# Kernel optimization log

Hardware: AMD Instinct MI355X
Metric: run time of the kernel (lower is better)

The kernel has to match this reference:

```python
import jax, jax.numpy as jnp
import numpy as np

B, DIM, H, W = 8, 128, 96, 96
EPS = 1e-5  # torch LayerNorm default


def setup_inputs() -> dict:
    key = jax.random.key(0)
    ks = jax.random.split(key, 4)
    d = DIM
    return {
        "x": jax.random.normal(ks[0], (B, d, H, W), jnp.float32),
        "W_in": jax.random.normal(ks[1], (2 * d, d), jnp.float32) * (d ** -0.5),
        "b_in": jnp.zeros((2 * d,), jnp.float32),
        "dw_w": jax.random.normal(ks[2], (d, 1, 7), jnp.float32) * 0.3,
        "dw_b": jnp.zeros((d,), jnp.float32),
        "gamma": jnp.ones((d,), jnp.float32),
        "beta": jnp.zeros((d,), jnp.float32),
        "W_out": jax.random.normal(ks[3], (d, d), jnp.float32) * (d ** -0.5),
        "b_out": jnp.zeros((d,), jnp.float32),
    }


def _mixer(x, W_in, b_in, dw_w, dw_b, gamma, beta, W_out, b_out):
    # x: (N, L, C). LinearStateSpace1D fallback mixer.
    d = x.shape[-1]
    uv = x @ W_in.T + b_in                      # (N, L, 2C)
    u, v = jnp.split(uv, 2, axis=-1)            # torch .chunk(2, -1)
    u = jax.nn.silu(u)
    v = jnp.swapaxes(v, 1, 2)                   # (N, C, L)
    v = jax.lax.conv_general_dilated(
        v, dw_w, window_strides=(1,), padding=[(3, 3)],
        dimension_numbers=("NCH", "OIH", "NCH"), feature_group_count=d,
    ) + dw_b[None, :, None]
    v = jax.nn.silu(jnp.swapaxes(v, 1, 2))      # (N, L, C)
    y = u * v
    mu = jnp.mean(y, axis=-1, keepdims=True)
    var = jnp.mean((y - mu) ** 2, axis=-1, keepdims=True)
    y = (y - mu) * jax.lax.rsqrt(var + EPS) * gamma + beta
    return y @ W_out.T + b_out


def reference(x, W_in, b_in, dw_w, dw_b, gamma, beta, W_out, b_out):
    Bc, C, Hh, Ww = x.shape
    L = Hh * Ww
    # 4-direction expand: lr, tb, rl (flip lr), bt (flip tb) -> stack on batch
    s_lr = jnp.transpose(x, (0, 2, 3, 1)).reshape(Bc, L, C)
    s_tb = jnp.transpose(x, (0, 3, 2, 1)).reshape(Bc, L, C)
    seqs = jnp.concatenate([s_lr, s_tb, s_lr[:, ::-1], s_tb[:, ::-1]], axis=0)
    y = _mixer(seqs, W_in, b_in, dw_w, dw_b, gamma, beta, W_out, b_out)
    y_lr, y_tb, y_rl, y_bt = jnp.split(y, 4, axis=0)
    y_rl = y_rl[:, ::-1]
    y_bt = y_bt[:, ::-1]
    m_lr = jnp.transpose(y_lr.reshape(Bc, Hh, Ww, C), (0, 3, 1, 2))
    m_rl = jnp.transpose(y_rl.reshape(Bc, Hh, Ww, C), (0, 3, 1, 2))
    m_tb = jnp.transpose(y_tb.reshape(Bc, Ww, Hh, C), (0, 3, 2, 1))
    m_bt = jnp.transpose(y_bt.reshape(Bc, Ww, Hh, C), (0, 3, 2, 1))
    return (m_lr + m_tb + m_rl + m_bt) * 0.25
```

## Files before the change

kernel.cpp:

```cpp
#include <hip/hip_runtime.h>

#define BB 8
#define HH 96
#define WW 96
#define LL 9216
#define EPSF 1e-5f

typedef __attribute__((ext_vector_type(8))) short short8;
typedef __attribute__((ext_vector_type(4))) float f32x4;
typedef __attribute__((ext_vector_type(2))) float f32x2;
typedef __attribute__((ext_vector_type(4))) unsigned int uint32x4;
typedef unsigned short ushort_t;
typedef unsigned int uint32;

__device__ __forceinline__ float silu_f(float x){
    return x * __builtin_amdgcn_rcpf(1.0f + __expf(-x));
}
__device__ __forceinline__ ushort_t f2bf(float f){
    uint32 u = __float_as_uint(f);
    u += 0x7FFFu + ((u >> 16) & 1u);
    return (ushort_t)(u >> 16);
}
__device__ __forceinline__ float bf2f(short h){
    return __uint_as_float(((uint32)(ushort_t)h) << 16);
}
__device__ __forceinline__ uint32 pack2(float a, float b){
    return (uint32)f2bf(a) | ((uint32)f2bf(b) << 16);
}

__global__ __launch_bounds__(256) void k_prep(const float* __restrict__ Win,
        const float* __restrict__ Wout, const float* __restrict__ dw_w,
        ushort_t* __restrict__ W2, ushort_t* __restrict__ WO2,
        float* __restrict__ dwT){
    int i = blockIdx.x * 256 + threadIdx.x;
    {
        int e = i & 7, ln = (i >> 3) & 63, ks = (i >> 9) & 3, of = i >> 11;
        W2[i] = f2bf(Win[(of*16 + (ln & 15))*128 + ks*32 + (ln >> 4)*8 + e]);
    }
    if (i < 16384){
        int e = i & 7, ln = (i >> 3) & 63, ks = (i >> 9) & 3, of = i >> 11;
        WO2[i] = f2bf(Wout[(of*16 + (ln & 15))*128 + ks*32 + (ln >> 4)*8 + e]);
    }
    if (i < 896){
        int j = i >> 7, c = i & 127;
        dwT[i] = dw_w[c*7 + j];
    }
}

__global__ __launch_bounds__(256) void k_gemmA(const float* __restrict__ x,
        const ushort_t* __restrict__ W2, const float* __restrict__ b_in,
        ushort_t* __restrict__ UV){
    __shared__ __align__(16) char unia[34816];
    float (*xt)[65] = (float(*)[65])unia;
    ushort_t* ec = (ushort_t*)unia;
    __shared__ __align__(16) ushort_t xtile[64 * 128];

    const int b = blockIdx.y, l0 = blockIdx.x * 64, tid = threadIdx.x;
    const int wv = tid >> 6, lane = tid & 63;
    const int lo = lane & 15, hi = lane >> 4;

    #pragma unroll
    for (int k = 0; k < 32; ++k){
        int c = (tid >> 6) + k * 4;
        xt[c][lane] = x[((size_t)(b * 128 + c)) * LL + l0 + lane];
    }
    __syncthreads();
    #pragma unroll
    for (int p = 0; p < 16; ++p){
        int l = (tid >> 6) + p * 4;
        uint32 v = pack2(xt[2 * lane][l], xt[2 * lane + 1][l]);
        *(uint32*)((char*)xtile + l * 256 + ((lane * 4) ^ ((l & 7) << 4))) = v;
    }
    __syncthreads();

    const f32x4 zero = {0.f, 0.f, 0.f, 0.f};
    f32x4 acc[4][4];
    #pragma unroll
    for (int om = 0; om < 4; ++om)
        #pragma unroll
        for (int lf = 0; lf < 4; ++lf) acc[om][lf] = zero;

    #pragma unroll
    for (int ks = 0; ks < 4; ++ks){
        short8 af[4], bfr[4];
        #pragma unroll
        for (int om = 0; om < 4; ++om)
            af[om] = *(const short8*)(W2 + (size_t)(((wv*4 + om)*4 + ks)*64 + lane)*8);
        #pragma unroll
        for (int lf = 0; lf < 4; ++lf){
            int tok = lf * 16 + lo;
            bfr[lf] = *(const short8*)((char*)xtile + tok * 256 +
                        ((ks * 64 + hi * 16) ^ ((tok & 7) << 4)));
        }
        #pragma unroll
        for (int om = 0; om < 4; ++om)
            #pragma unroll
            for (int lf = 0; lf < 4; ++lf)
                acc[om][lf] = __builtin_amdgcn_mfma_f32_16x16x32_bf16(af[om], bfr[lf], acc[om][lf], 0, 0, 0);
    }
    __syncthreads();

    #pragma unroll
    for (int om = 0; om < 4; ++om){
        int obase = wv * 64 + om * 16 + hi * 4;
        f32x4 bia = *(const f32x4*)(b_in + obase);
        const bool isU = (wv < 2);
        #pragma unroll
        for (int lf = 0; lf < 4; ++lf){
            #pragma unroll
            for (int r = 0; r < 4; ++r){
                float v = acc[om][lf][r] + bia[r];
                if (isU) v = silu_f(v);
                ec[(obase + r) * 68 + lf * 16 + lo] = f2bf(v);
            }
        }
    }
    __syncthreads();

    const int r8 = tid >> 5, c32 = tid & 31;
    #pragma unroll
    for (int p = 0; p < 32; ++p){
        int row = r8 + p * 8;
        int col = c32 * 2;
        uint32 v = *(const uint32*)(ec + row * 68 + col);
        *(uint32*)(UV + ((size_t)(b * 256 + row)) * LL + l0 + col) = v;
    }
}

__device__ __forceinline__ float tbfly8(float (&x)[8], int lane){
    const int t0 = lane & 1, t1 = (lane >> 1) & 1, t2 = (lane >> 2) & 1;
    float y[4], z[2];
    #pragma unroll
    for (int j = 0; j < 4; ++j){
        float keep = t0 ? x[2*j+1] : x[2*j];
        float send = t0 ? x[2*j]   : x[2*j+1];
        y[j] = keep + __shfl_xor(send, 1);
    }
    #pragma unroll
    for (int j = 0; j < 2; ++j){
        float keep = t1 ? y[2*j+1] : y[2*j];
        float send = t1 ? y[2*j]   : y[2*j+1];
        z[j] = keep + __shfl_xor(send, 2);
    }
    float keep = t2 ? z[1] : z[0];
    float send = t2 ? z[0] : z[1];
    return keep + __shfl_xor(send, 4);
}

__global__ __launch_bounds__(512, 4) void k_mixout(const ushort_t* __restrict__ UV,
        const float* __restrict__ dwT, const float* __restrict__ dw_b,
        const float* __restrict__ gamma, const float* __restrict__ beta,
        const ushort_t* __restrict__ WO2, const float* __restrict__ b_out,
        float* __restrict__ out){
    __shared__ __align__(16) float red[8][32][12];
    __shared__ float tot[32 * 6];
    __shared__ __align__(16) char ytile[32 * 288];

    const int flat = blockIdx.y * 288 + blockIdx.x;
    const int nf = (flat & 7) * 288 + (flat >> 3);
    const int b  = nf / 288;
    const int m0 = (nf % 288) * 32;

    const int tid  = threadIdx.x;
    const int lane = tid & 63;
    const int wv   = tid >> 6;
    const int cl   = lane & 15;
    const int tg   = lane >> 4;
    const int c0   = wv * 16 + cl;
    const int m8   = m0 + tg * 8;
    const int h    = m8 / WW;
    const int w0g  = m8 - h * WW;

    const ushort_t* vrow = UV + ((size_t)(b * 256 + 128) + c0) * LL + m8;

    short8 u8  = *(const short8*)(UV + ((size_t)(b * 256) + c0) * LL + m8);
    short8 WBm = *(const short8*)(vrow);
    short8 WA  = *(const short8*)(vrow - 8);
    short8 WC  = *(const short8*)(vrow + 8);
    short8 g8[6];
    bool inb[6];
    #pragma unroll
    for (int r = 0; r < 6; ++r){
        const int dd = (r < 3) ? (r - 3) : (r - 2);
        const int hd = h + dd;
        inb[r] = (hd >= 0) && (hd < HH);
        g8[r] = *(const short8*)(vrow + 96 * dd);
    }
    float cw[7];
    #pragma unroll
    for (int j = 0; j < 7; ++j) cw[j] = dwT[j * 128 + c0];
    const float bias = dw_b[c0];

    float ya[8], yb[8], yc[8], yd[8];
    float Sa, Qa, Sb, Qb, Sc, Qc, Sd, Qd;

    {
        float f[14];
        #pragma unroll
        for (int k = 0; k < 14; ++k){
            int e = 5 + k;
            f[k] = bf2f(e < 8 ? WA[e] : (e < 16 ? WBm[e - 8] : WC[e - 16]));
        }
        if (m8 == 0){ f[0] = 0.f; f[1] = 0.f; f[2] = 0.f; }
        if (m8 == LL - 8){ f[11] = 0.f; f[12] = 0.f; f[13] = 0.f; }
        float qa[8], qb[8];
        #pragma unroll
        for (int i = 0; i < 8; ++i){
            float caf = bias, cbw = bias;
            #pragma unroll
            for (int j = 0; j < 7; ++j){
                caf = fmaf(cw[j],     f[i + j], caf);
                cbw = fmaf(cw[6 - j], f[i + j], cbw);
            }
            float uu = bf2f(u8[i]);
            ya[i] = uu * silu_f(caf);
            yb[i] = uu * silu_f(cbw);
            qa[i] = ya[i] * ya[i];
            qb[i] = yb[i] * yb[i];
        }
        Sa = tbfly8(ya, lane); Sa += __shfl_xor(Sa, 8);
        Qa = tbfly8(qa, lane); Qa += __shfl_xor(Qa, 8);
        Sb = tbfly8(yb, lane); Sb += __shfl_xor(Sb, 8);
        Qb = tbfly8(qb, lane); Qb += __shfl_xor(Qb, 8);
    }

    {
        float caf[8], cbw[8];
        #pragma unroll
        for (int i = 0; i < 8; ++i){
            float v0 = bf2f(WBm[i]);
            caf[i] = fmaf(cw[3], v0, bias);
            cbw[i] = caf[i];
        }
        #pragma unroll
        for (int r = 0; r < 6; ++r){
            const int dd = (r < 3) ? (r - 3) : (r - 2);
            const int j  = dd + 3;
            float gv[8];
            if (inb[r]){
                #pragma unroll
                for (int i = 0; i < 8; ++i) gv[i] = bf2f(g8[r][i]);
            } else {
                const int hd = h + dd;
                const int del = (hd < 0) ? (LL - 1) : (1 - LL);
                #pragma unroll
                for (int i = 0; i < 8; ++i){
                    int q = (w0g + i) * HH + hd;
                    bool ok = (unsigned)q < (unsigned)LL;
                    gv[i] = ok ? bf2f(vrow[96 * dd + del + i]) : 0.f;
                }
            }
            #pragma unroll
            for (int i = 0; i < 8; ++i){
                caf[i] = fmaf(cw[j],     gv[i], caf[i]);
                cbw[i] = fmaf(cw[6 - j], gv[i], cbw[i]);
            }
        }
        float qc[8], qd[8];
        #pragma unroll
        for (int i = 0; i < 8; ++i){
            float uu = bf2f(u8[i]);
            yc[i] = uu * silu_f(caf[i]);
            yd[i] = uu * silu_f(cbw[i]);
            qc[i] = yc[i] * yc[i];
            qd[i] = yd[i] * yd[i];
        }
        Sc = tbfly8(yc, lane); Sc += __shfl_xor(Sc, 8);
        Qc = tbfly8(qc, lane); Qc += __shfl_xor(Qc, 8);
        Sd = tbfly8(yd, lane); Sd += __shfl_xor(Sd, 8);
        Qd = tbfly8(qd, lane); Qd += __shfl_xor(Qd, 8);
    }

    {
        const int tok32 = tg * 8 + (lane & 7);
        const int halfp = (lane >> 3) & 1;
        f32x4 stv;
        if (halfp){ stv[0] = Sc; stv[1] = Qc; stv[2] = Sd; stv[3] = Qd; }
        else      { stv[0] = Sa; stv[1] = Qa; stv[2] = Sb; stv[3] = Qb; }
        *(f32x4*)(&red[wv][tok32][halfp * 4]) = stv;
    }
    __syncthreads();
    if (tid < 32){
        f32x4 s0 = {0.f, 0.f, 0.f, 0.f}, s1 = {0.f, 0.f, 0.f, 0.f};
        #pragma unroll
        for (int w2 = 0; w2 < 8; ++w2){
            s0 += *(const f32x4*)(&red[w2][tid][0]);
            s1 += *(const f32x4*)(&red[w2][tid][4]);
        }
        const float inv = 1.f / 128.f;
        float mua = s0[0] * inv, ra = __builtin_amdgcn_rsqf(s0[1] * inv - mua * mua + EPSF);
        float mub = s0[2] * inv, rb = __builtin_amdgcn_rsqf(s0[3] * inv - mub * mub + EPSF);
        float muc = s1[0] * inv, rc = __builtin_amdgcn_rsqf(s1[1] * inv - muc * muc + EPSF);
        float mud = s1[2] * inv, rd = __builtin_amdgcn_rsqf(s1[3] * inv - mud * mud + EPSF);
        float C = mua * ra + mub * rb + muc * rc + mud * rd;
        tot[tid * 6 + 0] = ra; tot[tid * 6 + 1] = rb;
        tot[tid * 6 + 2] = rc; tot[tid * 6 + 3] = rd;
        tot[tid * 6 + 4] = C;
    }
    __syncthreads();

    {
        const float g4 = 0.25f * gamma[c0];
        const float be = beta[c0];
        #pragma unroll
        for (int i = 0; i < 8; ++i){
            int tok = tg * 8 + i;
            f32x2 r01 = *(const f32x2*)(&tot[tok * 6 + 0]);
            f32x2 r23 = *(const f32x2*)(&tot[tok * 6 + 2]);
            float C   = tot[tok * 6 + 4];
            float v = fmaf(ya[i], r01[0], fmaf(yb[i], r01[1],
                      fmaf(yc[i], r23[0], fmaf(yd[i], r23[1], -C))));
            int swz = ((tok & 7) ^ (tok >> 3)) << 4;
            *(ushort_t*)(ytile + tok * 288 + ((c0 * 2) ^ swz)) =
                f2bf(fmaf(g4, v, be));
        }
    }
    __syncthreads();

    const int lo = lane & 15, hi = lane >> 4;
    const int ow = wv;
    const f32x4 zero = {0.f, 0.f, 0.f, 0.f};
    f32x4 acc[2] = {zero, zero};
    #pragma unroll
    for (int ks = 0; ks < 4; ++ks){
        short8 af = *(const short8*)(WO2 + (size_t)((ow * 4 + ks) * 64 + lane) * 8);
        #pragma unroll
        for (int t2 = 0; t2 < 2; ++t2){
            int tok = t2 * 16 + lo;
            int swz = ((tok & 7) ^ (tok >> 3)) << 4;
            short8 bfr = *(const short8*)(ytile + tok * 288 +
                            ((ks * 64 + hi * 16) ^ swz));
            acc[t2] = __builtin_amdgcn_mfma_f32_16x16x32_bf16(af, bfr, acc[t2], 0, 0, 0);
        }
    }
    {
        f32x4 bia = *(const f32x4*)(b_out + ow * 16 + hi * 4);
        #pragma unroll
        for (int t2 = 0; t2 < 2; ++t2){
            int l = m0 + t2 * 16 + lo;
            #pragma unroll
            for (int r = 0; r < 4; ++r){
                int o = ow * 16 + hi * 4 + r;
                out[((size_t)(b * 128 + o)) * LL + l] = acc[t2][r] + bia[r];
            }
        }
    }
}

extern "C" void kernel_launch(void* const* d_in, const int* in_sizes, int n_in,
                              void* d_out, int out_size, void* d_ws, size_t ws_size,
                              hipStream_t stream) {
    const float* x     = (const float*)d_in[0];
    const float* W_in  = (const float*)d_in[1];
    const float* b_in  = (const float*)d_in[2];
    const float* dw_w  = (const float*)d_in[3];
    const float* dw_b  = (const float*)d_in[4];
    const float* gamma = (const float*)d_in[5];
    const float* beta  = (const float*)d_in[6];
    const float* W_out = (const float*)d_in[7];
    const float* b_out = (const float*)d_in[8];
    float* out = (float*)d_out;

    ushort_t* UV  = (ushort_t*)d_ws;
    ushort_t* W2  = UV + (size_t)BB * 256 * LL + 32;
    ushort_t* WO2 = W2 + 256 * 128;
    float*    dwT = (float*)(WO2 + 128 * 128);

    k_prep<<<128, 256, 0, stream>>>(W_in, W_out, dw_w, W2, WO2, dwT);

    dim3 gA(LL / 64, BB);
    k_gemmA<<<gA, 256, 0, stream>>>(x, W2, b_in, UV);

    dim3 gM(288, BB);
    k_mixout<<<gM, 512, 0, stream>>>(UV, dwT, dw_b, gamma, beta,
                                     WO2, b_out, out);
}
```

Baseline: 77.86 us.

## Remap mixout threads so each wave owns tokens, reducing LayerNorm in-wave

Each block now runs 256 threads instead of 512. Each wave handles 8 tokens across all 128 channels, with every lane processing two channels. The LayerNorm statistics are therefore reduced entirely with cross-lane shuffles, which removes the shared-memory reduction buffers and two block barriers. In exchange each thread holds twice the loaded data and accumulators, and each wave now computes two output-row MFMA tiles. The loads of UV rows become per-lane strided across channels rather than channel-contiguous, which may change coalescing behaviour. Relies on a pack2 helper presumed defined in the unseen part of the file.

```diff
diff --git a/kernel.cpp b/kernel.cpp
--- a/kernel.cpp
+++ b/kernel.cpp
@@ -147,14 +147,20 @@
     return keep + __shfl_xor(send, 4);
 }
 
-__global__ __launch_bounds__(512, 4) void k_mixout(const ushort_t* __restrict__ UV,
+__device__ __forceinline__ float wred8(float (&x)[8], int lane){
+    float s = tbfly8(x, lane);
+    s += __shfl_xor(s, 8);
+    s += __shfl_xor(s, 16);
+    s += __shfl_xor(s, 32);
+    return s;
+}
+
+__global__ __launch_bounds__(256, 3) void k_mixout(const ushort_t* __restrict__ UV,
         const float* __restrict__ dwT, const float* __restrict__ dw_b,
         const float* __restrict__ gamma, const float* __restrict__ beta,
         const ushort_t* __restrict__ WO2, const float* __restrict__ b_out,
         float* __restrict__ out){
-    __shared__ __align__(16) float red[8][32][12];
-    __shared__ float tot[32 * 6];
-    __shared__ __align__(16) char ytile[32 * 288];
+    __shared__ __align__(16) char ytile[32 * 256];
 
     const int flat = blockIdx.y * 288 + blockIdx.x;
     const int nf = (flat & 7) * 288 + (flat >> 3);
@@ -164,72 +170,70 @@
     const int tid  = threadIdx.x;
     const int lane = tid & 63;
     const int wv   = tid >> 6;
-    const int cl   = lane & 15;
-    const int tg   = lane >> 4;
-    const int c0   = wv * 16 + cl;
-    const int m8   = m0 + tg * 8;
+    const int cs   = lane;
+    const int m8   = m0 + wv * 8;
     const int h    = m8 / WW;
     const int w0g  = m8 - h * WW;
 
-    const ushort_t* vrow = UV + ((size_t)(b * 256 + 128) + c0) * LL + m8;
-
-    short8 u8  = *(const short8*)(UV + ((size_t)(b * 256) + c0) * LL + m8);
-    short8 WBm = *(const short8*)(vrow);
-    short8 WA  = *(const short8*)(vrow - 8);
-    short8 WC  = *(const short8*)(vrow + 8);
-    short8 g8[6];
+    const ushort_t* vrow[2];
+    vrow[0] = UV + ((size_t)(b * 256 + 128) + 2 * cs) * LL + m8;
+    vrow[1] = vrow[0] + LL;
+
+    short8 u8v[2], WBv[2], WAv[2], WCv[2], g8v[2][6];
+    #pragma unroll
+    for (int ch = 0; ch < 2; ++ch){
+        u8v[ch] = *(const short8*)(UV + ((size_t)(b * 256) + 2 * cs + ch) * LL + m8);
+        WBv[ch] = *(const short8*)(vrow[ch]);
+        WAv[ch] = *(const short8*)(vrow[ch] - 8);
+        WCv[ch] = *(const short8*)(vrow[ch] + 8);
+    }
     bool inb[6];
     #pragma unroll
     for (int r = 0; r < 6; ++r){
         const int dd = (r < 3) ? (r - 3) : (r - 2);
         const int hd = h + dd;
         inb[r] = (hd >= 0) && (hd < HH);
-        g8[r] = *(const short8*)(vrow + 96 * dd);
-    }
-    float cw[7];
-    #pragma unroll
-    for (int j = 0; j < 7; ++j) cw[j] = dwT[j * 128 + c0];
-    const float bias = dw_b[c0];
-
-    float ya[8], yb[8], yc[8], yd[8];
-    float Sa, Qa, Sb, Qb, Sc, Qc, Sd, Qd;
-
-    {
+        g8v[0][r] = *(const short8*)(vrow[0] + 96 * dd);
+        g8v[1][r] = *(const short8*)(vrow[1] + 96 * dd);
+    }
+    f32x2 cw2[7];
+    #pragma unroll
+    for (int j = 0; j < 7; ++j) cw2[j] = *(const f32x2*)(dwT + j * 128 + 2 * cs);
+    const f32x2 bias2 = *(const f32x2*)(dw_b + 2 * cs);
+
+    float ya[2][8], yb[2][8], yc[2][8], yd[2][8];
+
+    #pragma unroll
+    for (int ch = 0; ch < 2; ++ch){
         float f[14];
         #pragma unroll
         for (int k = 0; k < 14; ++k){
             int e = 5 + k;
-            f[k] = bf2f(e < 8 ? WA[e] : (e < 16 ? WBm[e - 8] : WC[e - 16]));
+            f[k] = bf2f(e < 8 ? WAv[ch][e] : (e < 16 ? WBv[ch][e - 8] : WCv[ch][e - 16]));
         }
         if (m8 == 0){ f[0] = 0.f; f[1] = 0.f; f[2] = 0.f; }
         if (m8 == LL - 8){ f[11] = 0.f; f[12] = 0.f; f[13] = 0.f; }
-        float qa[8], qb[8];
         #pragma unroll
         for (int i = 0; i < 8; ++i){
-            float caf = bias, cbw = bias;
+            float caf = bias2[ch], cbw = bias2[ch];
             #pragma unroll
             for (int j = 0; j < 7; ++j){
-                caf = fmaf(cw[j],     f[i + j], caf);
-                cbw = fmaf(cw[6 - j], f[i + j], cbw);
+                caf = fmaf(cw2[j][ch],     f[i + j], caf);
+                cbw = fmaf(cw2[6 - j][ch], f[i + j], cbw);
             }
-            float uu = bf2f(u8[i]);
-            ya[i] = uu * silu_f(caf);
-            yb[i] = uu * silu_f(cbw);
-            qa[i] = ya[i] * ya[i];
-            qb[i] = yb[i] * yb[i];
-        }
-        Sa = tbfly8(ya, lane); Sa += __shfl_xor(Sa, 8);
-        Qa = tbfly8(qa, lane); Qa += __shfl_xor(Qa, 8);
-        Sb = tbfly8(yb, lane); Sb += __shfl_xor(Sb, 8);
-        Qb = tbfly8(qb, lane); Qb += __shfl_xor(Qb, 8);
-    }
-
-    {
+            float uu = bf2f(u8v[ch][i]);
+            ya[ch][i] = uu * silu_f(caf);
+            yb[ch][i] = uu * silu_f(cbw);
+        }
+    }
+
+    #pragma unroll
+    for (int ch = 0; ch < 2; ++ch){
         float caf[8], cbw[8];
         #pragma unroll
         for (int i = 0; i < 8; ++i){
-            float v0 = bf2f(WBm[i]);
-            caf[i] = fmaf(cw[3], v0, bias);
+            float v0 = bf2f(WBv[ch][i]);
+            caf[i] = fmaf(cw2[3][ch], v0, bias2[ch]);
             cbw[i] = caf[i];
         }
         #pragma unroll
@@ -239,7 +243,7 @@
             float gv[8];
             if (inb[r]){
                 #pragma unroll
-                for (int i = 0; i < 8; ++i) gv[i] = bf2f(g8[r][i]);
+                for (int i = 0; i < 8; ++i) gv[i] = bf2f(g8v[ch][r][i]);
             } else {
                 const int hd = h + dd;
                 const int del = (hd < 0) ? (LL - 1) : (1 - LL);
@@ -247,102 +251,104 @@
                 for (int i = 0; i < 8; ++i){
                     int q = (w0g + i) * HH + hd;
                     bool ok = (unsigned)q < (unsigned)LL;
-                    gv[i] = ok ? bf2f(vrow[96 * dd + del + i]) : 0.f;
+                    gv[i] = ok ? bf2f(vrow[ch][96 * dd + del + i]) : 0.f;
                 }
             }
             #pragma unroll
             for (int i = 0; i < 8; ++i){
-                caf[i] = fmaf(cw[j],     gv[i], caf[i]);
-                cbw[i] = fmaf(cw[6 - j], gv[i], cbw[i]);
+                caf[i] = fmaf(cw2[j][ch],     gv[i], caf[i]);
+                cbw[i] = fmaf(cw2[6 - j][ch], gv[i], cbw[i]);
             }
         }
-        float qc[8], qd[8];
         #pragma unroll
         for (int i = 0; i < 8; ++i){
-            float uu = bf2f(u8[i]);
-            yc[i] = uu * silu_f(caf[i]);
-            yd[i] = uu * silu_f(cbw[i]);
-            qc[i] = yc[i] * yc[i];
-            qd[i] = yd[i] * yd[i];
-        }
-        Sc = tbfly8(yc, lane); Sc += __shfl_xor(Sc, 8);
-        Qc = tbfly8(qc, lane); Qc += __shfl_xor(Qc, 8);
-        Sd = tbfly8(yd, lane); Sd += __shfl_xor(Sd, 8);
-        Qd = tbfly8(qd, lane); Qd += __shfl_xor(Qd, 8);
-    }
-
+            float uu = bf2f(u8v[ch][i]);
+            yc[ch][i] = uu * silu_f(caf[i]);
+            yd[ch][i] = uu * silu_f(cbw[i]);
+        }
+    }
+
+    float Sa, Qa, Sb, Qb, Sc, Qc, Sd, Qd;
     {
-        const int tok32 = tg * 8 + (lane & 7);
-        const int halfp = (lane >> 3) & 1;
-        f32x4 stv;
-        if (halfp){ stv[0] = Sc; stv[1] = Qc; stv[2] = Sd; stv[3] = Qd; }
-        else      { stv[0] = Sa; stv[1] = Qa; stv[2] = Sb; stv[3] = Qb; }
-        *(f32x4*)(&red[wv][tok32][halfp * 4]) = stv;
-    }
-    __syncthreads();
-    if (tid < 32){
-        f32x4 s0 = {0.f, 0.f, 0.f, 0.f}, s1 = {0.f, 0.f, 0.f, 0.f};
-        #pragma unroll
-        for (int w2 = 0; w2 < 8; ++w2){
-            s0 += *(const f32x4*)(&red[w2][tid][0]);
-            s1 += *(const f32x4*)(&red[w2][tid][4]);
-        }
-        const float inv = 1.f / 128.f;
-        float mua = s0[0] * inv, ra = __builtin_amdgcn_rsqf(s0[1] * inv - mua * mua + EPSF);
-        float mub = s0[2] * inv, rb = __builtin_amdgcn_rsqf(s0[3] * inv - mub * mub + EPSF);
-        float muc = s1[0] * inv, rc = __builtin_amdgcn_rsqf(s1[1] * inv - muc * muc + EPSF);
-        float mud = s1[2] * inv, rd = __builtin_amdgcn_rsqf(s1[3] * inv - mud * mud + EPSF);
-        float C = mua * ra + mub * rb + muc * rc + mud * rd;
-        tot[tid * 6 + 0] = ra; tot[tid * 6 + 1] = rb;
-        tot[tid * 6 + 2] = rc; tot[tid * 6 + 3] = rd;
-        tot[tid * 6 + 4] = C;
-    }
-    __syncthreads();
+        float s[8], q[8];
+        #pragma unroll
+        for (int i = 0; i < 8; ++i){ s[i] = ya[0][i] + ya[1][i];
+            q[i] = fmaf(ya[0][i], ya[0][i], ya[1][i] * ya[1][i]); }
+        Sa = wred8(s, lane); Qa = wred8(q, lane);
+        #pragma unroll
+        for (int i = 0; i < 8; ++i){ s[i] = yb[0][i] + yb[1][i];
+            q[i] = fmaf(yb[0][i], yb[0][i], yb[1][i] * yb[1][i]); }
+        Sb = wred8(s, lane); Qb = wred8(q, lane);
+        #pragma unroll
+        for (int i = 0; i < 8; ++i){ s[i] = yc[0][i] + yc[1][i];
+            q[i] = fmaf(yc[0][i], yc[0][i], yc[1][i] * yc[1][i]); }
+        Sc = wred8(s, lane); Qc = wred8(q, lane);
+        #pragma unroll
+        for (int i = 0; i < 8; ++i){ s[i] = yd[0][i] + yd[1][i];
+            q[i] = fmaf(yd[0][i], yd[0][i], yd[1][i] * yd[1][i]); }
+        Sd = wred8(s, lane); Qd = wred8(q, lane);
+    }
+    const float inv = 1.f / 128.f;
+    float mua = Sa * inv, ra = __builtin_amdgcn_rsqf(Qa * inv - mua * mua + EPSF);
+    float mub = Sb * inv, rb = __builtin_amdgcn_rsqf(Qb * inv - mub * mub + EPSF);
+    float muc = Sc * inv, rc = __builtin_amdgcn_rsqf(Qc * inv - muc * muc + EPSF);
+    float mud = Sd * inv, rd = __builtin_amdgcn_rsqf(Qd * inv - mud * mud + EPSF);
+    float Cst = fmaf(mua, ra, fmaf(mub, rb, fmaf(muc, rc, mud * rd)));
 
     {
-        const float g4 = 0.25f * gamma[c0];
-        const float be = beta[c0];
+        f32x2 g2 = *(const f32x2*)(gamma + 2 * cs);
+        f32x2 e2 = *(const f32x2*)(beta + 2 * cs);
+        const float g40 = 0.25f * g2[0], g41 = 0.25f * g2[1];
         #pragma unroll
         for (int i = 0; i < 8; ++i){
-            int tok = tg * 8 + i;
-            f32x2 r01 = *(const f32x2*)(&tot[tok * 6 + 0]);
-            f32x2 r23 = *(const f32x2*)(&tot[tok * 6 + 2]);
-            float C   = tot[tok * 6 + 4];
-            float v = fmaf(ya[i], r01[0], fmaf(yb[i], r01[1],
-                      fmaf(yc[i], r23[0], fmaf(yd[i], r23[1], -C))));
+            float rai = __shfl(ra, i, 8);
+            float rbi = __shfl(rb, i, 8);
+            float rci = __shfl(rc, i, 8);
+            float rdi = __shfl(rd, i, 8);
+            float Ci  = __shfl(Cst, i, 8);
+            float v0 = fmaf(ya[0][i], rai, fmaf(yb[0][i], rbi,
+                       fmaf(yc[0][i], rci, fmaf(yd[0][i], rdi, -Ci))));
+            float v1 = fmaf(ya[1][i], rai, fmaf(yb[1][i], rbi,
+                       fmaf(yc[1][i], rci, fmaf(yd[1][i], rdi, -Ci))));
+            uint32 pk = pack2(fmaf(g40, v0, e2[0]), fmaf(g41, v1, e2[1]));
+            int tok = wv * 8 + i;
             int swz = ((tok & 7) ^ (tok >> 3)) << 4;
-            *(ushort_t*)(ytile + tok * 288 + ((c0 * 2) ^ swz)) =
-                f2bf(fmaf(g4, v, be));
+            *(uint32*)(ytile + tok * 256 + ((cs * 4) ^ swz)) = pk;
         }
     }
     __syncthreads();
 
     const int lo = lane & 15, hi = lane >> 4;
-    const int ow = wv;
     const f32x4 zero = {0.f, 0.f, 0.f, 0.f};
-    f32x4 acc[2] = {zero, zero};
+    f32x4 acc[2][2];
+    acc[0][0] = zero; acc[0][1] = zero; acc[1][0] = zero; acc[1][1] = zero;
     #pragma unroll
     for (int ks = 0; ks < 4; ++ks){
-        short8 af = *(const short8*)(WO2 + (size_t)((ow * 4 + ks) * 64 + lane) * 8);
+        short8 af[2];
+        #pragma unroll
+        for (int om = 0; om < 2; ++om)
+            af[om] = *(const short8*)(WO2 + (size_t)(((wv*2 + om)*4 + ks)*64 + lane)*8);
         #pragma unroll
         for (int t2 = 0; t2 < 2; ++t2){
             int tok = t2 * 16 + lo;
             int swz = ((tok & 7) ^ (tok >> 3)) << 4;
-            short8 bfr = *(const short8*)(ytile + tok * 288 +
+            short8 bfr = *(const short8*)(ytile + tok * 256 +
                             ((ks * 64 + hi * 16) ^ swz));
-            acc[t2] = __builtin_amdgcn_mfma_f32_16x16x32_bf16(af, bfr, acc[t2], 0, 0, 0);
-        }
-    }
-    {
-        f32x4 bia = *(const f32x4*)(b_out + ow * 16 + hi * 4);
+            #pragma unroll
+            for (int om = 0; om < 2; ++om)
+                acc[om][t2] = __builtin_amdgcn_mfma_f32_16x16x32_bf16(af[om], bfr, acc[om][t2], 0, 0, 0);
+        }
+    }
+    #pragma unroll
+    for (int om = 0; om < 2; ++om){
+        int ob = (wv * 2 + om) * 16 + hi * 4;
+        f32x4 bia = *(const f32x4*)(b_out + ob);
         #pragma unroll
         for (int t2 = 0; t2 < 2; ++t2){
             int l = m0 + t2 * 16 + lo;
             #pragma unroll
-            for (int r = 0; r < 4; ++r){
-                int o = ow * 16 + hi * 4 + r;
-                out[((size_t)(b * 128 + o)) * LL + l] = acc[t2][r] + bia[r];
-            }
+            for (int r = 0; r < 4; ++r)
+                out[((size_t)(b * 128 + ob + r)) * LL + l] = acc[om][t2][r] + bia[r];
         }
     }
 }
@@ -372,6 +378,6 @@
     k_gemmA<<<gA, 256, 0, stream>>>(x, W2, b_in, UV);
 
     dim3 gM(288, BB);
-    k_mixout<<<gM, 512, 0, stream>>>(UV, dwT, dw_b, gamma, beta,
+    k_mixout<<<gM, 256, 0, stream>>>(UV, dwT, dw_b, gamma, beta,
                                      WO2, b_out, out);
 }
```

After: 95.02 us. +22.0%, slower.
